# Kernel optimization log

Hardware: AMD Instinct MI355X
Metric: run time of the kernel (lower is better)

Reference implementation:

```python
import jax, jax.numpy as jnp
import numpy as np

WINDOW = 256          # causal local window: each token attends to itself + 255 previous
SCALE = 64 ** -0.5    # head_size ** -0.5 (softmax_scale default)
NEG_INF = -1e30


def setup_inputs() -> dict:
    key = jax.random.key(0)
    kq, kk, kv = jax.random.split(key, 3)
    B, S, H, D = 2, 8192, 16, 64
    q = jax.random.normal(kq, (B, S, H, D), dtype=jnp.float32)
    k = jax.random.normal(kk, (B, S, H, D), dtype=jnp.float32)
    v = jax.random.normal(kv, (B, S, H, D), dtype=jnp.float32)
    return {"q": q, "k": k, "v": v}


def local_attention(q, k, v, window=WINDOW, scale=SCALE):
    """Causal sliding-window attention. q,k,v: [B,S,H,D], S % window == 0.

    Block-local formulation: query block n attends to key blocks n-1 and n,
    with a banded mask so each query sees exactly `window` tokens (incl. self).
    Never materializes an [S,S] score matrix.
    """
    B, S, H, D = q.shape
    W = window
    nb = S // W
    qb = q.reshape(B, nb, W, H, D)
    kb = k.reshape(B, nb, W, H, D)
    vb = v.reshape(B, nb, W, H, D)
    # previous key/value block (zero-padded for block 0)
    kprev = jnp.concatenate([jnp.zeros_like(kb[:, :1]), kb[:, :-1]], axis=1)
    vprev = jnp.concatenate([jnp.zeros_like(vb[:, :1]), vb[:, :-1]], axis=1)
    k2 = jnp.concatenate([kprev, kb], axis=2)  # [B,nb,2W,H,D]
    v2 = jnp.concatenate([vprev, vb], axis=2)

    # scores: [B,nb,H,W,2W]
    scores = jnp.einsum('bnqhd,bnkhd->bnhqk', qb, k2) * scale

    qi = jnp.arange(W)[:, None]        # local query index within block
    ki = jnp.arange(2 * W)[None, :]    # key index within [prev|cur] blocks
    rel = qi + W - ki                  # distance: 0 == self, positive == past
    band = (rel >= 0) & (rel < W)      # [W,2W] causal window band
    # block 0 has no real previous block: only current-block keys valid
    blk = jnp.arange(nb)[:, None, None]
    mask = band[None] & ((blk > 0) | (ki >= W)[None])   # [nb,W,2W]

    scores = jnp.where(mask[None, :, None], scores, NEG_INF)
    p = jax.nn.softmax(scores, axis=-1)
    out = jnp.einsum('bnhqk,bnkhd->bnqhd', p, v2)
    return out.reshape(B, S, H, D)


def reference(q, k, v):
    return local_attention(q, k, v)
```

## Files before the change

kernel.cpp:

```cpp
#include <hip/hip_runtime.h>

typedef __attribute__((ext_vector_type(8))) short short8;
typedef __attribute__((ext_vector_type(4))) float f32x4;
typedef __attribute__((ext_vector_type(2))) unsigned u32x2;
typedef __attribute__((ext_vector_type(4))) unsigned u32x4;

#define SCL2 0.18033688011112042f

__device__ __forceinline__ unsigned pk2(float lo, float hi) {
  unsigned r;
  asm("v_cvt_pk_bf16_f32 %0, %1, %2" : "=v"(r) : "v"(lo), "v"(hi));
  return r;
}

__device__ __forceinline__ short8 pk8(float4 a, float4 b) {
  u32x4 u = { pk2(a.x, a.y), pk2(a.z, a.w), pk2(b.x, b.y), pk2(b.z, b.w) };
  return __builtin_bit_cast(short8, u);
}

__global__ __launch_bounds__(256, 3)
void lattn(const float* __restrict__ Qg, const float* __restrict__ Kg,
           const float* __restrict__ Vg, float* __restrict__ Og) {
  constexpr int S = 8192, H = 16, RS = H * 64;
  __shared__ __align__(16) unsigned char smem[32768];
  unsigned char* Klds = smem;
  unsigned char* Vlds = smem + 8192;

  const int tid = threadIdx.x;
  const int l = tid & 63, w = tid >> 6, g = l >> 4, l15 = l & 15;
  unsigned char* Plds = smem + 16384 + w * 4096;

  const int wg = ((blockIdx.x & 7) << 8) + (blockIdx.x >> 3);
  const int n = wg & 63, h = (wg >> 6) & 15, b = wg >> 10;

  const float* Qp = Qg + (size_t)b * S * RS + h * 64;
  const float* Kp = Kg + (size_t)b * S * RS + h * 64;
  const float* Vp = Vg + (size_t)b * S * RS + h * 64;
  float*       Op = Og + (size_t)b * S * RS + h * 64;

  const int wq0 = 32 * w;
  const int qg0 = n * 128 + wq0;

  short8 qf[2][2];
#pragma unroll
  for (int nr = 0; nr < 2; ++nr) {
    const float* qrow = Qp + (size_t)(qg0 + 16 * nr + l15) * RS;
#pragma unroll
    for (int ks = 0; ks < 2; ++ks) {
      float4 a = *(const float4*)(qrow + g * 8 + 32 * ks);
      float4 c = *(const float4*)(qrow + g * 8 + 32 * ks + 4);
      a.x *= SCL2; a.y *= SCL2; a.z *= SCL2; a.w *= SCL2;
      c.x *= SCL2; c.y *= SCL2; c.z *= SCL2; c.w *= SCL2;
      qf[ks][nr] = pk8(a, c);
    }
  }

  f32x4 acc[2][4];
#pragma unroll
  for (int i = 0; i < 2; ++i)
#pragma unroll
    for (int j = 0; j < 4; ++j) acc[i][j] = f32x4{0.f, 0.f, 0.f, 0.f};
  float m_run[2] = {-1e20f, -1e20f};
  float l_run[2] = {0.f, 0.f};

  const int kvb = n * 128 - 256;
  const int t0 = (n == 0) ? 4 : ((n == 1) ? 2 : 0);

  for (int t = t0; t < 6; ++t) {
    __syncthreads();
#pragma unroll
    for (int cc = 0; cc < 2; ++cc) {
      int cid = tid + (cc << 8);
      int r = cid >> 3, ch = cid & 7;
      const float* src = Kp + (size_t)(kvb + t * 64 + r) * RS + ch * 8;
      float4 a = *(const float4*)(src);
      float4 c = *(const float4*)(src + 4);
      *(short8*)(Klds + r * 128 + ((ch ^ (r & 7)) << 4)) = pk8(a, c);
    }
#pragma unroll
    for (int cc = 0; cc < 2; ++cc) {
      int cid = tid + (cc << 8);
      int d = cid & 63, kc = cid >> 6;
      const float* src = Vp + (size_t)(kvb + t * 64 + kc * 8) * RS + d;
      float f0 = src[0], f1 = src[RS], f2 = src[2 * RS], f3 = src[3 * RS];
      float f4 = src[4 * RS], f5 = src[5 * RS], f6 = src[6 * RS], f7 = src[7 * RS];
      u32x4 u = { pk2(f0, f1), pk2(f2, f3), pk2(f4, f5), pk2(f6, f7) };
      *(short8*)(Vlds + d * 128 + ((kc ^ (d & 7)) << 4)) = __builtin_bit_cast(short8, u);
    }
    __syncthreads();

    if (64 * t + 63 > wq0 && 64 * t <= wq0 + 287) {
      const bool noMask = (64 * t >= wq0 + 32) && (64 * t + 63 <= wq0 + 256);

      f32x4 s[4][2];
#pragma unroll
      for (int i = 0; i < 4; ++i)
#pragma unroll
        for (int j = 0; j < 2; ++j) s[i][j] = f32x4{0.f, 0.f, 0.f, 0.f};
#pragma unroll
      for (int ks = 0; ks < 2; ++ks) {
        short8 kf[4];
#pragma unroll
        for (int mr = 0; mr < 4; ++mr) {
          int r = mr * 16 + l15;
          kf[mr] = *(const short8*)(Klds + r * 128 + (((g + 4 * ks) ^ (r & 7)) << 4));
        }
#pragma unroll
        for (int mr = 0; mr < 4; ++mr)
#pragma unroll
          for (int nr = 0; nr < 2; ++nr)
            s[mr][nr] = __builtin_amdgcn_mfma_f32_16x16x32_bf16(kf[mr], qf[ks][nr],
                                                                s[mr][nr], 0, 0, 0);
      }

      float corrv[2];
#pragma unroll
      for (int nr = 0; nr < 2; ++nr) {
        int q = wq0 + 16 * nr + l15;
        float mx = -3e38f;
        if (noMask) {
#pragma unroll
          for (int mr = 0; mr < 4; ++mr)
#pragma unroll
            for (int reg = 0; reg < 4; ++reg) mx = fmaxf(mx, s[mr][nr][reg]);
        } else {
#pragma unroll
          for (int mr = 0; mr < 4; ++mr)
#pragma unroll
            for (int reg = 0; reg < 4; ++reg) {
              int koff = 64 * t + 16 * mr + 4 * g + reg;
              bool valid = (koff > q) && (koff <= q + 256);
              float sv = valid ? s[mr][nr][reg] : -1e30f;
              s[mr][nr][reg] = sv;
              mx = fmaxf(mx, sv);
            }
        }
        mx = fmaxf(mx, __shfl_xor(mx, 16));
        mx = fmaxf(mx, __shfl_xor(mx, 32));
        float mnew = fmaxf(m_run[nr], mx);
        float corr = exp2f(m_run[nr] - mnew);
        m_run[nr] = mnew;
        float sum = 0.f;
#pragma unroll
        for (int mr = 0; mr < 4; ++mr)
#pragma unroll
          for (int reg = 0; reg < 4; ++reg) {
            float p = exp2f(s[mr][nr][reg] - mnew);
            s[mr][nr][reg] = p;
            sum += p;
          }
        sum += __shfl_xor(sum, 16);
        sum += __shfl_xor(sum, 32);
        l_run[nr] = l_run[nr] * corr + sum;
        corrv[nr] = corr;
      }
#pragma unroll
      for (int nr = 0; nr < 2; ++nr)
#pragma unroll
        for (int mr = 0; mr < 4; ++mr) {
          int q = 16 * nr + l15;
          int cb = 2 * mr + (g >> 1);
          int off = q * 128 + ((cb ^ (q & 7)) << 4) + ((g & 1) << 3);
          u32x2 pw = { pk2(s[mr][nr][0], s[mr][nr][1]),
                       pk2(s[mr][nr][2], s[mr][nr][3]) };
          *(u32x2*)(Plds + off) = pw;
        }
#pragma unroll
      for (int mq = 0; mq < 2; ++mq)
#pragma unroll
        for (int reg = 0; reg < 4; ++reg) {
          float c = __shfl(corrv[mq], 4 * g + reg, 16);
#pragma unroll
          for (int nd = 0; nd < 4; ++nd) acc[mq][nd][reg] *= c;
        }
      asm volatile("s_waitcnt lgkmcnt(0)" ::: "memory");

#pragma unroll
      for (int ks = 0; ks < 2; ++ks) {
        short8 pf[2], vf[4];
#pragma unroll
        for (int mq = 0; mq < 2; ++mq) {
          int q = 16 * mq + l15;
          pf[mq] = *(const short8*)(Plds + q * 128 + (((g + 4 * ks) ^ (q & 7)) << 4));
        }
#pragma unroll
        for (int nd = 0; nd < 4; ++nd) {
          int d = 16 * nd + l15;
          vf[nd] = *(const short8*)(Vlds + d * 128 + (((g + 4 * ks) ^ (d & 7)) << 4));
        }
#pragma unroll
        for (int mq = 0; mq < 2; ++mq)
#pragma unroll
          for (int nd = 0; nd < 4; ++nd)
            acc[mq][nd] = __builtin_amdgcn_mfma_f32_16x16x32_bf16(pf[mq], vf[nd],
                                                                  acc[mq][nd], 0, 0, 0);
      }
    }
  }

  float linv[2] = {1.0f / l_run[0], 1.0f / l_run[1]};
#pragma unroll
  for (int mq = 0; mq < 2; ++mq)
#pragma unroll
    for (int reg = 0; reg < 4; ++reg) {
      float li = __shfl(linv[mq], 4 * g + reg, 16);
      int qrow = qg0 + 16 * mq + 4 * g + reg;
      float* orow = Op + (size_t)qrow * RS;
#pragma unroll
      for (int nd = 0; nd < 4; ++nd)
        orow[16 * nd + l15] = acc[mq][nd][reg] * li;
    }
}

extern "C" void kernel_launch(void* const* d_in, const int* in_sizes, int n_in,
                              void* d_out, int out_size, void* d_ws, size_t ws_size,
                              hipStream_t stream) {
  (void)in_sizes; (void)n_in; (void)d_ws; (void)ws_size; (void)out_size;
  const float* q = (const float*)d_in[0];
  const float* k = (const float*)d_in[1];
  const float* v = (const float*)d_in[2];
  float* o = (float*)d_out;
  dim3 grid(2 * 16 * 64);
  dim3 block(256);
  lattn<<<grid, block, 0, stream>>>(q, k, v, o);
}
```

Baseline: 254.2 us.

## Double-buffer K/V tiles with register prefetch to overlap loads and compute

New measurement: 867.1 us. 241% more time.

```diff
diff --git a/kernel.cpp b/kernel.cpp
--- a/kernel.cpp
+++ b/kernel.cpp
@@ -22,13 +22,15 @@
 void lattn(const float* __restrict__ Qg, const float* __restrict__ Kg,
            const float* __restrict__ Vg, float* __restrict__ Og) {
   constexpr int S = 8192, H = 16, RS = H * 64;
-  __shared__ __align__(16) unsigned char smem[32768];
-  unsigned char* Klds = smem;
-  unsigned char* Vlds = smem + 8192;
+  __shared__ __align__(16) unsigned char smem[49152];
+  unsigned char* Kb0 = smem;
+  unsigned char* Vb0 = smem + 8192;
+  unsigned char* Kb1 = smem + 16384;
+  unsigned char* Vb1 = smem + 24576;
 
   const int tid = threadIdx.x;
   const int l = tid & 63, w = tid >> 6, g = l >> 4, l15 = l & 15;
-  unsigned char* Plds = smem + 16384 + w * 4096;
+  unsigned char* Plds = smem + 32768 + w * 4096;
 
   const int wg = ((blockIdx.x & 7) << 8) + (blockIdx.x >> 3);
   const int n = wg & 63, h = (wg >> 6) & 15, b = wg >> 10;
@@ -40,6 +42,11 @@
 
   const int wq0 = 32 * w;
   const int qg0 = n * 128 + wq0;
+
+  const int kr_ = tid >> 3, kch = tid & 7;
+  const int vd = tid & 63, vkc0 = tid >> 6;
+  const int kvb = n * 128 - 256;
+  const int t0 = (n == 0) ? 4 : ((n == 1) ? 2 : 0);
 
   short8 qf[2][2];
 #pragma unroll
@@ -63,139 +70,153 @@
   float m_run[2] = {-1e20f, -1e20f};
   float l_run[2] = {0.f, 0.f};
 
-  const int kvb = n * 128 - 256;
-  const int t0 = (n == 0) ? 4 : ((n == 1) ? 2 : 0);
-
-  for (int t = t0; t < 6; ++t) {
+  auto issueT = [&](float4* kr, float* vr, int t) {
+#pragma unroll
+    for (int cc = 0; cc < 2; ++cc) {
+      const float* ks_ = Kp + (size_t)(kvb + t * 64 + kr_ + 32 * cc) * RS + kch * 8;
+      kr[2 * cc]     = *(const float4*)(ks_);
+      kr[2 * cc + 1] = *(const float4*)(ks_ + 4);
+      const float* vs = Vp + (size_t)(kvb + t * 64 + (vkc0 + 4 * cc) * 8) * RS + vd;
+#pragma unroll
+      for (int i = 0; i < 8; ++i) vr[8 * cc + i] = vs[(size_t)i * RS];
+    }
+  };
+  auto writeT = [&](unsigned char* Kb, unsigned char* Vb, const float4* kr, const float* vr) {
+#pragma unroll
+    for (int cc = 0; cc < 2; ++cc) {
+      int r = kr_ + 32 * cc;
+      *(short8*)(Kb + r * 128 + ((kch ^ (r & 7)) << 4)) = pk8(kr[2 * cc], kr[2 * cc + 1]);
+      int kc = vkc0 + 4 * cc;
+      u32x4 u = { pk2(vr[8 * cc + 0], vr[8 * cc + 1]), pk2(vr[8 * cc + 2], vr[8 * cc + 3]),
+                  pk2(vr[8 * cc + 4], vr[8 * cc + 5]), pk2(vr[8 * cc + 6], vr[8 * cc + 7]) };
+      *(short8*)(Vb + vd * 128 + ((kc ^ (vd & 7)) << 4)) = __builtin_bit_cast(short8, u);
+    }
+  };
+
+  auto computeT = [&](const unsigned char* Kb, const unsigned char* Vb, int t) {
+    if (!(64 * t + 63 > wq0 && 64 * t <= wq0 + 287)) return;
+    const bool noMask = (64 * t >= wq0 + 32) && (64 * t + 63 <= wq0 + 256);
+
+    f32x4 s[4][2];
+#pragma unroll
+    for (int i = 0; i < 4; ++i)
+#pragma unroll
+      for (int j = 0; j < 2; ++j) s[i][j] = f32x4{0.f, 0.f, 0.f, 0.f};
+#pragma unroll
+    for (int ks = 0; ks < 2; ++ks) {
+      short8 kf[4];
+#pragma unroll
+      for (int mr = 0; mr < 4; ++mr) {
+        int r = mr * 16 + l15;
+        kf[mr] = *(const short8*)(Kb + r * 128 + (((g + 4 * ks) ^ (r & 7)) << 4));
+      }
+#pragma unroll
+      for (int mr = 0; mr < 4; ++mr)
+#pragma unroll
+        for (int nr = 0; nr < 2; ++nr)
+          s[mr][nr] = __builtin_amdgcn_mfma_f32_16x16x32_bf16(kf[mr], qf[ks][nr],
+                                                              s[mr][nr], 0, 0, 0);
+    }
+
+    float corrv[2];
+#pragma unroll
+    for (int nr = 0; nr < 2; ++nr) {
+      int q = wq0 + 16 * nr + l15;
+      float mx = -3e38f;
+      if (noMask) {
+#pragma unroll
+        for (int mr = 0; mr < 4; ++mr)
+#pragma unroll
+          for (int reg = 0; reg < 4; ++reg) mx = fmaxf(mx, s[mr][nr][reg]);
+      } else {
+#pragma unroll
+        for (int mr = 0; mr < 4; ++mr)
+#pragma unroll
+          for (int reg = 0; reg < 4; ++reg) {
+            int koff = 64 * t + 16 * mr + 4 * g + reg;
+            bool valid = (koff > q) && (koff <= q + 256);
+            float sv = valid ? s[mr][nr][reg] : -1e30f;
+            s[mr][nr][reg] = sv;
+            mx = fmaxf(mx, sv);
+          }
+      }
+      mx = fmaxf(mx, __shfl_xor(mx, 16));
+      mx = fmaxf(mx, __shfl_xor(mx, 32));
+      float mnew = fmaxf(m_run[nr], mx);
+      float corr = exp2f(m_run[nr] - mnew);
+      m_run[nr] = mnew;
+      float sum = 0.f;
+#pragma unroll
+      for (int mr = 0; mr < 4; ++mr)
+#pragma unroll
+        for (int reg = 0; reg < 4; ++reg) {
+          float p = exp2f(s[mr][nr][reg] - mnew);
+          s[mr][nr][reg] = p;
+          sum += p;
+        }
+      sum += __shfl_xor(sum, 16);
+      sum += __shfl_xor(sum, 32);
+      l_run[nr] = l_run[nr] * corr + sum;
+      corrv[nr] = corr;
+    }
+#pragma unroll
+    for (int nr = 0; nr < 2; ++nr)
+#pragma unroll
+      for (int mr = 0; mr < 4; ++mr) {
+        int q = 16 * nr + l15;
+        int cb = 2 * mr + (g >> 1);
+        int off = q * 128 + ((cb ^ (q & 7)) << 4) + ((g & 1) << 3);
+        u32x2 pw = { pk2(s[mr][nr][0], s[mr][nr][1]),
+                     pk2(s[mr][nr][2], s[mr][nr][3]) };
+        *(u32x2*)(Plds + off) = pw;
+      }
+#pragma unroll
+    for (int mq = 0; mq < 2; ++mq)
+#pragma unroll
+      for (int reg = 0; reg < 4; ++reg) {
+        float c = __shfl(corrv[mq], 4 * g + reg, 16);
+#pragma unroll
+        for (int nd = 0; nd < 4; ++nd) acc[mq][nd][reg] *= c;
+      }
+    asm volatile("s_waitcnt lgkmcnt(0)" ::: "memory");
+
+#pragma unroll
+    for (int ks = 0; ks < 2; ++ks) {
+      short8 pf[2], vf[4];
+#pragma unroll
+      for (int mq = 0; mq < 2; ++mq) {
+        int q = 16 * mq + l15;
+        pf[mq] = *(const short8*)(Plds + q * 128 + (((g + 4 * ks) ^ (q & 7)) << 4));
+      }
+#pragma unroll
+      for (int nd = 0; nd < 4; ++nd) {
+        int d = 16 * nd + l15;
+        vf[nd] = *(const short8*)(Vb + d * 128 + (((g + 4 * ks) ^ (d & 7)) << 4));
+      }
+#pragma unroll
+      for (int mq = 0; mq < 2; ++mq)
+#pragma unroll
+        for (int nd = 0; nd < 4; ++nd)
+          acc[mq][nd] = __builtin_amdgcn_mfma_f32_16x16x32_bf16(pf[mq], vf[nd],
+                                                                acc[mq][nd], 0, 0, 0);
+    }
+  };
+
+  float4 krA[4]; float vrA[16];
+  float4 krB[4]; float vrB[16];
+  issueT(krA, vrA, t0);
+
+  for (int tp = t0 >> 1; tp < 3; ++tp) {
+    const int te = 2 * tp;
+    writeT(Kb0, Vb0, krA, vrA);
     __syncthreads();
-#pragma unroll
-    for (int cc = 0; cc < 2; ++cc) {
-      int cid = tid + (cc << 8);
-      int r = cid >> 3, ch = cid & 7;
-      const float* src = Kp + (size_t)(kvb + t * 64 + r) * RS + ch * 8;
-      float4 a = *(const float4*)(src);
-      float4 c = *(const float4*)(src + 4);
-      *(short8*)(Klds + r * 128 + ((ch ^ (r & 7)) << 4)) = pk8(a, c);
-    }
-#pragma unroll
-    for (int cc = 0; cc < 2; ++cc) {
-      int cid = tid + (cc << 8);
-      int d = cid & 63, kc = cid >> 6;
-      const float* src = Vp + (size_t)(kvb + t * 64 + kc * 8) * RS + d;
-      float f0 = src[0], f1 = src[RS], f2 = src[2 * RS], f3 = src[3 * RS];
-      float f4 = src[4 * RS], f5 = src[5 * RS], f6 = src[6 * RS], f7 = src[7 * RS];
-      u32x4 u = { pk2(f0, f1), pk2(f2, f3), pk2(f4, f5), pk2(f6, f7) };
-      *(short8*)(Vlds + d * 128 + ((kc ^ (d & 7)) << 4)) = __builtin_bit_cast(short8, u);
-    }
+    issueT(krB, vrB, te + 1);
+    computeT(Kb0, Vb0, te);
+
+    writeT(Kb1, Vb1, krB, vrB);
     __syncthreads();
-
-    if (64 * t + 63 > wq0 && 64 * t <= wq0 + 287) {
-      const bool noMask = (64 * t >= wq0 + 32) && (64 * t + 63 <= wq0 + 256);
-
-      f32x4 s[4][2];
-#pragma unroll
-      for (int i = 0; i < 4; ++i)
-#pragma unroll
-        for (int j = 0; j < 2; ++j) s[i][j] = f32x4{0.f, 0.f, 0.f, 0.f};
-#pragma unroll
-      for (int ks = 0; ks < 2; ++ks) {
-        short8 kf[4];
-#pragma unroll
-        for (int mr = 0; mr < 4; ++mr) {
-          int r = mr * 16 + l15;
-          kf[mr] = *(const short8*)(Klds + r * 128 + (((g + 4 * ks) ^ (r & 7)) << 4));
-        }
-#pragma unroll
-        for (int mr = 0; mr < 4; ++mr)
-#pragma unroll
-          for (int nr = 0; nr < 2; ++nr)
-            s[mr][nr] = __builtin_amdgcn_mfma_f32_16x16x32_bf16(kf[mr], qf[ks][nr],
-                                                                s[mr][nr], 0, 0, 0);
-      }
-
-      float corrv[2];
-#pragma unroll
-      for (int nr = 0; nr < 2; ++nr) {
-        int q = wq0 + 16 * nr + l15;
-        float mx = -3e38f;
-        if (noMask) {
-#pragma unroll
-          for (int mr = 0; mr < 4; ++mr)
-#pragma unroll
-            for (int reg = 0; reg < 4; ++reg) mx = fmaxf(mx, s[mr][nr][reg]);
-        } else {
-#pragma unroll
-          for (int mr = 0; mr < 4; ++mr)
-#pragma unroll
-            for (int reg = 0; reg < 4; ++reg) {
-              int koff = 64 * t + 16 * mr + 4 * g + reg;
-              bool valid = (koff > q) && (koff <= q + 256);
-              float sv = valid ? s[mr][nr][reg] : -1e30f;
-              s[mr][nr][reg] = sv;
-              mx = fmaxf(mx, sv);
-            }
-        }
-        mx = fmaxf(mx, __shfl_xor(mx, 16));
-        mx = fmaxf(mx, __shfl_xor(mx, 32));
-        float mnew = fmaxf(m_run[nr], mx);
-        float corr = exp2f(m_run[nr] - mnew);
-        m_run[nr] = mnew;
-        float sum = 0.f;
-#pragma unroll
-        for (int mr = 0; mr < 4; ++mr)
-#pragma unroll
-          for (int reg = 0; reg < 4; ++reg) {
-            float p = exp2f(s[mr][nr][reg] - mnew);
-            s[mr][nr][reg] = p;
-            sum += p;
-          }
-        sum += __shfl_xor(sum, 16);
-        sum += __shfl_xor(sum, 32);
-        l_run[nr] = l_run[nr] * corr + sum;
-        corrv[nr] = corr;
-      }
-#pragma unroll
-      for (int nr = 0; nr < 2; ++nr)
-#pragma unroll
-        for (int mr = 0; mr < 4; ++mr) {
-          int q = 16 * nr + l15;
-          int cb = 2 * mr + (g >> 1);
-          int off = q * 128 + ((cb ^ (q & 7)) << 4) + ((g & 1) << 3);
-          u32x2 pw = { pk2(s[mr][nr][0], s[mr][nr][1]),
-                       pk2(s[mr][nr][2], s[mr][nr][3]) };
-          *(u32x2*)(Plds + off) = pw;
-        }
-#pragma unroll
-      for (int mq = 0; mq < 2; ++mq)
-#pragma unroll
-        for (int reg = 0; reg < 4; ++reg) {
-          float c = __shfl(corrv[mq], 4 * g + reg, 16);
-#pragma unroll
-          for (int nd = 0; nd < 4; ++nd) acc[mq][nd][reg] *= c;
-        }
-      asm volatile("s_waitcnt lgkmcnt(0)" ::: "memory");
-
-#pragma unroll
-      for (int ks = 0; ks < 2; ++ks) {
-        short8 pf[2], vf[4];
-#pragma unroll
-        for (int mq = 0; mq < 2; ++mq) {
-          int q = 16 * mq + l15;
-          pf[mq] = *(const short8*)(Plds + q * 128 + (((g + 4 * ks) ^ (q & 7)) << 4));
-        }
-#pragma unroll
-        for (int nd = 0; nd < 4; ++nd) {
-          int d = 16 * nd + l15;
-          vf[nd] = *(const short8*)(Vlds + d * 128 + (((g + 4 * ks) ^ (d & 7)) << 4));
-        }
-#pragma unroll
-        for (int mq = 0; mq < 2; ++mq)
-#pragma unroll
-          for (int nd = 0; nd < 4; ++nd)
-            acc[mq][nd] = __builtin_amdgcn_mfma_f32_16x16x32_bf16(pf[mq], vf[nd],
-                                                                  acc[mq][nd], 0, 0, 0);
-      }
-    }
+    if (te + 2 < 6) issueT(krA, vrA, te + 2);
+    computeT(Kb1, Vb1, te + 1);
   }
 
   float linv[2] = {1.0f / l_run[0], 1.0f / l_run[1]};
```

## Prefetch next K tile into registers and overlap V loads with QK softmax

Applied to the files above, without the earlier changes.

After: 257.7 us. Within noise of the previous version (+1.4%).

```diff
diff --git a/kernel.cpp b/kernel.cpp
--- a/kernel.cpp
+++ b/kernel.cpp
@@ -17,6 +17,14 @@
   u32x4 u = { pk2(a.x, a.y), pk2(a.z, a.w), pk2(b.x, b.y), pk2(b.z, b.w) };
   return __builtin_bit_cast(short8, u);
 }
+
+#define LDS_BARRIER()                                        \
+  do {                                                       \
+    asm volatile("s_waitcnt lgkmcnt(0)" ::: "memory");       \
+    __builtin_amdgcn_sched_barrier(0);                       \
+    __builtin_amdgcn_s_barrier();                            \
+    __builtin_amdgcn_sched_barrier(0);                       \
+  } while (0)
 
 __global__ __launch_bounds__(256, 3)
 void lattn(const float* __restrict__ Qg, const float* __restrict__ Kg,
@@ -41,6 +49,11 @@
   const int wq0 = 32 * w;
   const int qg0 = n * 128 + wq0;
 
+  const int kr_ = tid >> 3, kch = tid & 7;
+  const int vd = tid & 63, vkc0 = tid >> 6;
+  const int kvb = n * 128 - 256;
+  const int t0 = (n == 0) ? 4 : ((n == 1) ? 2 : 0);
+
   short8 qf[2][2];
 #pragma unroll
   for (int nr = 0; nr < 2; ++nr) {
@@ -63,33 +76,42 @@
   float m_run[2] = {-1e20f, -1e20f};
   float l_run[2] = {0.f, 0.f};
 
-  const int kvb = n * 128 - 256;
-  const int t0 = (n == 0) ? 4 : ((n == 1) ? 2 : 0);
+  const float* kb0 = Kp + (size_t)(kvb + t0 * 64 + kr_) * RS + kch * 8;
+  float4 kc0 = *(const float4*)(kb0);
+  float4 kc1 = *(const float4*)(kb0 + 4);
+  float4 kc2 = *(const float4*)(kb0 + (size_t)32 * RS);
+  float4 kc3 = *(const float4*)(kb0 + (size_t)32 * RS + 4);
+  float4 kn0 = kc0, kn1 = kc1, kn2 = kc2, kn3 = kc3;
 
   for (int t = t0; t < 6; ++t) {
-    __syncthreads();
-#pragma unroll
-    for (int cc = 0; cc < 2; ++cc) {
-      int cid = tid + (cc << 8);
-      int r = cid >> 3, ch = cid & 7;
-      const float* src = Kp + (size_t)(kvb + t * 64 + r) * RS + ch * 8;
-      float4 a = *(const float4*)(src);
-      float4 c = *(const float4*)(src + 4);
-      *(short8*)(Klds + r * 128 + ((ch ^ (r & 7)) << 4)) = pk8(a, c);
-    }
-#pragma unroll
-    for (int cc = 0; cc < 2; ++cc) {
-      int cid = tid + (cc << 8);
-      int d = cid & 63, kc = cid >> 6;
-      const float* src = Vp + (size_t)(kvb + t * 64 + kc * 8) * RS + d;
-      float f0 = src[0], f1 = src[RS], f2 = src[2 * RS], f3 = src[3 * RS];
-      float f4 = src[4 * RS], f5 = src[5 * RS], f6 = src[6 * RS], f7 = src[7 * RS];
-      u32x4 u = { pk2(f0, f1), pk2(f2, f3), pk2(f4, f5), pk2(f6, f7) };
-      *(short8*)(Vlds + d * 128 + ((kc ^ (d & 7)) << 4)) = __builtin_bit_cast(short8, u);
-    }
-    __syncthreads();
-
-    if (64 * t + 63 > wq0 && 64 * t <= wq0 + 287) {
+    const float* vb0 = Vp + (size_t)(kvb + t * 64 + vkc0 * 8) * RS + vd;
+    const float* vb1 = vb0 + (size_t)32 * RS;
+    float vv0 = vb0[0],              vv1 = vb0[(size_t)1 * RS];
+    float vv2 = vb0[(size_t)2 * RS], vv3 = vb0[(size_t)3 * RS];
+    float vv4 = vb0[(size_t)4 * RS], vv5 = vb0[(size_t)5 * RS];
+    float vv6 = vb0[(size_t)6 * RS], vv7 = vb0[(size_t)7 * RS];
+    float vv8 = vb1[0],              vv9 = vb1[(size_t)1 * RS];
+    float vvA = vb1[(size_t)2 * RS], vvB = vb1[(size_t)3 * RS];
+    float vvC = vb1[(size_t)4 * RS], vvD = vb1[(size_t)5 * RS];
+    float vvE = vb1[(size_t)6 * RS], vvF = vb1[(size_t)7 * RS];
+
+    {
+      int r0 = kr_, r1 = kr_ + 32;
+      *(short8*)(Klds + r0 * 128 + ((kch ^ (r0 & 7)) << 4)) = pk8(kc0, kc1);
+      *(short8*)(Klds + r1 * 128 + ((kch ^ (r1 & 7)) << 4)) = pk8(kc2, kc3);
+    }
+    LDS_BARRIER();
+
+    if (t < 5) {
+      const float* kb = Kp + (size_t)(kvb + (t + 1) * 64 + kr_) * RS + kch * 8;
+      kn0 = *(const float4*)(kb);
+      kn1 = *(const float4*)(kb + 4);
+      kn2 = *(const float4*)(kb + (size_t)32 * RS);
+      kn3 = *(const float4*)(kb + (size_t)32 * RS + 4);
+    }
+
+    const bool active = (64 * t + 63 > wq0) && (64 * t <= wq0 + 287);
+    if (active) {
       const bool noMask = (64 * t >= wq0 + 32) && (64 * t + 63 <= wq0 + 256);
 
       f32x4 s[4][2];
@@ -173,8 +195,19 @@
 #pragma unroll
           for (int nd = 0; nd < 4; ++nd) acc[mq][nd][reg] *= c;
         }
-      asm volatile("s_waitcnt lgkmcnt(0)" ::: "memory");
-
+    }
+
+    {
+      u32x4 u0 = { pk2(vv0, vv1), pk2(vv2, vv3), pk2(vv4, vv5), pk2(vv6, vv7) };
+      int kc_ = vkc0;
+      *(short8*)(Vlds + vd * 128 + ((kc_ ^ (vd & 7)) << 4)) = __builtin_bit_cast(short8, u0);
+      u32x4 u1 = { pk2(vv8, vv9), pk2(vvA, vvB), pk2(vvC, vvD), pk2(vvE, vvF) };
+      kc_ = vkc0 + 4;
+      *(short8*)(Vlds + vd * 128 + ((kc_ ^ (vd & 7)) << 4)) = __builtin_bit_cast(short8, u1);
+    }
+    LDS_BARRIER();
+
+    if (active) {
 #pragma unroll
       for (int ks = 0; ks < 2; ++ks) {
         short8 pf[2], vf[4];
@@ -196,6 +229,7 @@
                                                                   acc[mq][nd], 0, 0, 0);
       }
     }
+    kc0 = kn0; kc1 = kn1; kc2 = kn2; kc3 = kn3;
   }
 
   float linv[2] = {1.0f / l_run[0], 1.0f / l_run[1]};
```
